# Optimization experiments

Measured on AMD Instinct MI355X. Metric: run time of the kernel, lower is better.

The kernel has to match this reference:

```python
import math
import jax, jax.numpy as jnp
import numpy as np

DN = ('NCHW', 'OIHW', 'NCHW')

def _conv2d(x, w, b, stride, padding='VALID'):
    y = jax.lax.conv_general_dilated(x, w, window_strides=stride, padding=padding,
                                     dimension_numbers=DN)
    return y + b[None, :, None, None]

def _same_padding_conv(x, w, b, s):
    # replicate torch same_padding_conv: ceil-mode SAME padding, then VALID conv
    H, W = x.shape[2], x.shape[3]
    kh, kw = w.shape[2], w.shape[3]
    out_h, out_w = math.ceil(H / s[0]), math.ceil(W / s[1])
    pad_h = max((out_h - 1) * s[0] + kh - H, 0)
    pad_w = max((out_w - 1) * s[1] + kw - W, 0)
    pt, pl = pad_h // 2, pad_w // 2
    x = jnp.pad(x, ((0, 0), (0, 0), (pt, pad_h - pt), (pl, pad_w - pl)))
    return _conv2d(x, w, b, s)

def _leaky(x):
    return jax.nn.leaky_relu(x, negative_slope=0.2)

def setup_inputs() -> dict:
    key = jax.random.key(0)
    ks = jax.random.split(key, 8)
    B, cin, cout, H, W = 2, 16, 24, 384, 1280
    fl = jax.random.normal(ks[0], (B, cin, H, W), jnp.float32)
    fr = jax.random.normal(ks[1], (B, cin, H, W), jnp.float32)
    w_em = jax.random.normal(ks[2], (cout, cin, 4, 4), jnp.float32) * 0.05
    b_em = jax.random.normal(ks[3], (cout,), jnp.float32) * 0.05
    w_rc = jax.random.normal(ks[4], (cout, cout, 1, 1), jnp.float32) * 0.1
    b_rc = jax.random.normal(ks[5], (cout,), jnp.float32) * 0.05
    w_tf = jax.random.normal(ks[6], (13, cout + 1, 1, 1), jnp.float32) * 0.1
    b_tf = jax.random.normal(ks[7], (13,), jnp.float32) * 0.05
    return {'feature_left': fl, 'feature_right': fr, 'max_disp': 64,
            'w_em': w_em, 'b_em': b_em, 'w_rc': w_rc, 'b_rc': b_rc,
            'w_tf': w_tf, 'b_tf': b_tf}

def reference(feature_left, feature_right, max_disp, w_em, b_em, w_rc, b_rc, w_tf, b_tf):
    # left branch: 4x4 conv, stride (4,4), VALID (torch default padding=0)
    fl = _leaky(_conv2d(_leaky(_conv2d(feature_left, w_em, b_em, (4, 4))), w_rc, b_rc, (1, 1)))
    # right branch: same-padding conv with stride (4,1) -> full width retained
    fr = _leaky(_conv2d(_leaky(_same_padding_conv(feature_right, w_em, b_em, (4, 1))), w_rc, b_rc, (1, 1)))
    B, C, Hq, Wq = fl.shape
    Wr = fr.shape[3]
    # clipped gather indices: idx[d, x] = clip(4*x - d + 1, 0, Wr-1)
    d = jnp.arange(max_disp)[:, None]          # [D,1]
    x = jnp.arange(Wq)[None, :]                # [1,Wq]
    idx = jnp.clip(4 * x - d + 1, 0, Wr - 1)   # [D,Wq]
    fr_g = jnp.take(fr, idx, axis=3)           # [B,C,H,D,Wq]
    # L1 cost over channels -> [B,D,H,Wq]
    cost_volume = jnp.sum(jnp.abs(fl[:, :, :, None, :] - fr_g), axis=1).transpose(0, 2, 1, 3)
    cost_f = jnp.min(cost_volume, axis=1, keepdims=True)                  # [B,1,H,Wq]
    d_init = jnp.argmin(cost_volume, axis=1, keepdims=True).astype(fl.dtype)
    p_init = jnp.concatenate([cost_f, fl], axis=1)
    p_init = _leaky(_conv2d(p_init, w_tf, b_tf, (1, 1)))                  # [B,13,H,Wq]
    z = jnp.zeros_like(d_init)
    out = jnp.concatenate([d_init, z, z, p_init], axis=1)                 # [B,16,H,Wq]
    return out, cost_volume
```

## Files before the change

kernel.cpp:

```cpp
#include <hip/hip_runtime.h>

#define B_   2
#define CIN  16
#define HIN  384
#define WIN  1280
#define CO   24
#define HQ   96
#define WL   320
#define WR   1280
#define DMAX 64

__device__ __forceinline__ float lk(float v) { return v >= 0.f ? v : 0.2f * v; }

__global__ __launch_bounds__(256) void k_left(
    const float* __restrict__ x, const float* __restrict__ w_em,
    const float* __restrict__ b_em, const float* __restrict__ w_rc,
    const float* __restrict__ b_rc, float* __restrict__ out)
{
    __shared__ float sw[CO * CIN * 16];
    __shared__ float swt[CO * CO];
    __shared__ float sbe[CO], sbr[CO];
    __shared__ float em[CO * 128];

    for (int i = threadIdx.x; i < CO * CIN * 16; i += 256) sw[i] = w_em[i];
    for (int i = threadIdx.x; i < CO * CO; i += 256) swt[i] = w_rc[(i % CO) * CO + (i / CO)];
    if (threadIdx.x < CO) { sbe[threadIdx.x] = b_em[threadIdx.x]; sbr[threadIdx.x] = b_rc[threadIdx.x]; }
    __syncthreads();

    const int t = threadIdx.x;
    const int half = t >> 7, pxl = t & 127;
    const int obase = half * 12;
    const int flat = blockIdx.x * 128 + pxl;
    const int j = flat % WL, h = (flat / WL) % HQ, b = flat / (WL * HQ);

    float acc[12];
#pragma unroll
    for (int oo = 0; oo < 12; ++oo) acc[oo] = sbe[obase + oo];

    for (int c = 0; c < CIN; ++c) {
#pragma unroll
        for (int kh = 0; kh < 4; ++kh) {
            const float4 v = *(const float4*)(x + ((size_t)(b * CIN + c) * HIN + 4 * h + kh) * WIN + 4 * j);
#pragma unroll
            for (int oo = 0; oo < 12; ++oo) {
                const float4 wv = *(const float4*)&sw[(((obase + oo) * CIN + c) * 4 + kh) * 4];
                acc[oo] += v.x * wv.x + v.y * wv.y + v.z * wv.z + v.w * wv.w;
            }
        }
    }
#pragma unroll
    for (int oo = 0; oo < 12; ++oo) em[(obase + oo) * 128 + pxl] = lk(acc[oo]);
    __syncthreads();

    float acc2[12];
#pragma unroll
    for (int oo = 0; oo < 12; ++oo) acc2[oo] = sbr[obase + oo];
    for (int c = 0; c < CO; ++c) {
        const float in_c = em[c * 128 + pxl];
#pragma unroll
        for (int oo = 0; oo < 12; ++oo) acc2[oo] += in_c * swt[c * CO + obase + oo];
    }
#pragma unroll
    for (int oo = 0; oo < 12; ++oo)
        out[((size_t)(b * CO + obase + oo) * HQ + h) * WL + j] = lk(acc2[oo]);
}

__global__ __launch_bounds__(256) void k_right(
    const float* __restrict__ x, const float* __restrict__ w_em,
    const float* __restrict__ b_em, const float* __restrict__ w_rc,
    const float* __restrict__ b_rc, float* __restrict__ out)
{
    __shared__ float sw[CO * CIN * 16];
    __shared__ float swt[CO * CO];
    __shared__ float sbe[CO], sbr[CO];
    __shared__ float em[CO * 256];

    for (int i = threadIdx.x; i < CO * CIN * 16; i += 256) sw[i] = w_em[i];
    for (int i = threadIdx.x; i < CO * CO; i += 256) swt[i] = w_rc[(i % CO) * CO + (i / CO)];
    if (threadIdx.x < CO) { sbe[threadIdx.x] = b_em[threadIdx.x]; sbr[threadIdx.x] = b_rc[threadIdx.x]; }
    __syncthreads();

    const int t = threadIdx.x;
    const int L = t & 63, quarter = t >> 6;
    const int obase = quarter * 6;
    const int row = blockIdx.x / 5, jbase = (blockIdx.x % 5) * 256;
    const int b = row / HQ, h = row % HQ;

    const bool vm1 = (jbase + 4 * L - 1) >= 0;
    const bool vp4 = (jbase + 4 * L + 4) < WIN;
    const bool vp5 = (jbase + 4 * L + 5) < WIN;
    const int  im1 = 4 * L - 1;
    const int  ip4 = 4 * L + 4;
    const int  ip5 = 4 * L + 5;

    float acc[4][6];
#pragma unroll
    for (int k = 0; k < 4; ++k)
#pragma unroll
        for (int oo = 0; oo < 6; ++oo) acc[k][oo] = sbe[obase + oo];

    for (int c = 0; c < CIN; ++c) {
#pragma unroll
        for (int kh = 0; kh < 4; ++kh) {
            const float* xr = x + ((size_t)(b * CIN + c) * HIN + 4 * h + kh) * WIN + jbase;
            const float4 v = *(const float4*)(xr + 4 * L);
            float in[7];
            in[0] = vm1 ? xr[im1] : 0.f;
            in[1] = v.x; in[2] = v.y; in[3] = v.z; in[4] = v.w;
            in[5] = vp4 ? xr[ip4] : 0.f;
            in[6] = vp5 ? xr[ip5] : 0.f;
#pragma unroll
            for (int oo = 0; oo < 6; ++oo) {
                const float4 wv = *(const float4*)&sw[(((obase + oo) * CIN + c) * 4 + kh) * 4];
#pragma unroll
                for (int k = 0; k < 4; ++k)
                    acc[k][oo] += in[k] * wv.x + in[k + 1] * wv.y + in[k + 2] * wv.z + in[k + 3] * wv.w;
            }
        }
    }
#pragma unroll
    for (int oo = 0; oo < 6; ++oo) {
        float4 st = make_float4(lk(acc[0][oo]), lk(acc[1][oo]), lk(acc[2][oo]), lk(acc[3][oo]));
        *(float4*)&em[(obase + oo) * 256 + 4 * L] = st;
    }
    __syncthreads();

    float acc2[CO];
#pragma unroll
    for (int o = 0; o < CO; ++o) acc2[o] = sbr[o];
    for (int c = 0; c < CO; ++c) {
        const float in_c = em[c * 256 + t];
#pragma unroll
        for (int o = 0; o < CO; ++o) acc2[o] += in_c * swt[c * CO + o];
    }
#pragma unroll
    for (int o = 0; o < CO; ++o)
        out[((size_t)(b * CO + o) * HQ + h) * WR + jbase + t] = lk(acc2[o]);
}

__global__ __launch_bounds__(320) void k_cost(
    const float* __restrict__ fl, const float* __restrict__ fr,
    const float* __restrict__ wtf, const float* __restrict__ btf,
    float* __restrict__ out, float* __restrict__ cost)
{
    __shared__ float frs[4 * 12 * 337];

    const int j = threadIdx.x;
    const int b = blockIdx.x / HQ, h = blockIdx.x % HQ;

    float acc[DMAX];
#pragma unroll
    for (int d = 0; d < DMAX; ++d) acc[d] = 0.f;

    for (int ch = 0; ch < 2; ++ch) {
        const int c0 = ch * 12;
        __syncthreads();
        for (int c = 0; c < 12; ++c) {
            const float* frow = fr + ((size_t)(b * CO + c0 + c) * HQ + h) * WR;
            const float4 v = *(const float4*)(frow + 4 * j);
            frs[(0 * 12 + c) * 337 + j + 16] = v.x;
            frs[(1 * 12 + c) * 337 + j + 16] = v.y;
            frs[(2 * 12 + c) * 337 + j + 16] = v.z;
            frs[(3 * 12 + c) * 337 + j + 16] = v.w;
            if (j >= 1 && j < 64)
                frs[((j & 3) * 12 + c) * 337 + (j >> 2)] = frow[0];
        }
        __syncthreads();

        for (int c = 0; c < 12; ++c) {
            const float flc = fl[((size_t)(b * CO + c0 + c) * HQ + h) * WL + j];
#pragma unroll
            for (int p = 0; p < 4; ++p) {
                const int dp0 = (1 - p) & 3;
                const int q0 = j + ((65 - dp0) >> 2);
                const int abase = (p * 12 + c) * 337 + q0;
#pragma unroll
                for (int i = 0; i < 16; ++i) {
                    const float v = frs[abase - i];
                    acc[dp0 + 4 * i] += fabsf(flc - v);
                }
            }
        }
    }

    float best = acc[0]; int bd = 0;
#pragma unroll
    for (int d = 1; d < DMAX; ++d)
        if (acc[d] < best) { best = acc[d]; bd = d; }

    const size_t cbase = ((size_t)b * DMAX * HQ + h) * WL + j;
#pragma unroll
    for (int d = 0; d < DMAX; ++d)
        cost[cbase + (size_t)d * (HQ * WL)] = acc[d];

    float flr[CO];
#pragma unroll
    for (int c = 0; c < CO; ++c) flr[c] = fl[((size_t)(b * CO + c) * HQ + h) * WL + j];

#pragma unroll
    for (int o = 0; o < 13; ++o) {
        float a = btf[o] + wtf[o * 25] * best;
#pragma unroll
        for (int c = 0; c < CO; ++c) a += wtf[o * 25 + 1 + c] * flr[c];
        out[((size_t)(b * 16 + 3 + o) * HQ + h) * WL + j] = lk(a);
    }
    out[((size_t)(b * 16 + 0) * HQ + h) * WL + j] = (float)bd;
    out[((size_t)(b * 16 + 1) * HQ + h) * WL + j] = 0.f;
    out[((size_t)(b * 16 + 2) * HQ + h) * WL + j] = 0.f;
}

extern "C" void kernel_launch(void* const* d_in, const int* in_sizes, int n_in,
                              void* d_out, int out_size, void* d_ws, size_t ws_size,
                              hipStream_t stream) {
    const float* fl_in = (const float*)d_in[0];
    const float* fr_in = (const float*)d_in[1];
    const float* w_em = (const float*)d_in[3];
    const float* b_em = (const float*)d_in[4];
    const float* w_rc = (const float*)d_in[5];
    const float* b_rc = (const float*)d_in[6];
    const float* w_tf = (const float*)d_in[7];
    const float* b_tf = (const float*)d_in[8];

    float* out  = (float*)d_out;
    float* cost = out + (size_t)B_ * 16 * HQ * WL;

    float* fl_ws = (float*)d_ws;
    float* fr_ws = fl_ws + (size_t)B_ * CO * HQ * WL;

    hipLaunchKernelGGL(k_left,  dim3(480), dim3(256), 0, stream,
                       fl_in, w_em, b_em, w_rc, b_rc, fl_ws);
    hipLaunchKernelGGL(k_right, dim3(960), dim3(256), 0, stream,
                       fr_in, w_em, b_em, w_rc, b_rc, fr_ws);
    hipLaunchKernelGGL(k_cost,  dim3(192), dim3(320), 0, stream,
                       fl_ws, fr_ws, w_tf, b_tf, out, cost);
}
```

Before: 278.0 us.

## Split cost kernel over disparity groups and column chunks; alias conv shared memory

The cost kernel now gives each thread 16 disparities instead of 64 and splits each row into 64-column chunks. This raises the grid from 192 to 960 blocks and cuts per-thread register pressure. A shared-memory argmin reduction then merges the four disparity groups before the 1x1 output conv. In exchange, each chunk redundantly loads some overlapping right-feature columns, and the conv kernels now reuse the weight shared buffer for intermediates to lower LDS use and raise occupancy.

```diff
diff --git a/kernel.cpp b/kernel.cpp
--- a/kernel.cpp
+++ b/kernel.cpp
@@ -17,12 +17,11 @@
     const float* __restrict__ b_em, const float* __restrict__ w_rc,
     const float* __restrict__ b_rc, float* __restrict__ out)
 {
-    __shared__ float sw[CO * CIN * 16];
+    __shared__ float smem[CO * CIN * 16];
     __shared__ float swt[CO * CO];
     __shared__ float sbe[CO], sbr[CO];
-    __shared__ float em[CO * 128];
-
-    for (int i = threadIdx.x; i < CO * CIN * 16; i += 256) sw[i] = w_em[i];
+
+    for (int i = threadIdx.x; i < CO * CIN * 16; i += 256) smem[i] = w_em[i];
     for (int i = threadIdx.x; i < CO * CO; i += 256) swt[i] = w_rc[(i % CO) * CO + (i / CO)];
     if (threadIdx.x < CO) { sbe[threadIdx.x] = b_em[threadIdx.x]; sbr[threadIdx.x] = b_rc[threadIdx.x]; }
     __syncthreads();
@@ -43,20 +42,21 @@
             const float4 v = *(const float4*)(x + ((size_t)(b * CIN + c) * HIN + 4 * h + kh) * WIN + 4 * j);
 #pragma unroll
             for (int oo = 0; oo < 12; ++oo) {
-                const float4 wv = *(const float4*)&sw[(((obase + oo) * CIN + c) * 4 + kh) * 4];
+                const float4 wv = *(const float4*)&smem[(((obase + oo) * CIN + c) * 4 + kh) * 4];
                 acc[oo] += v.x * wv.x + v.y * wv.y + v.z * wv.z + v.w * wv.w;
             }
         }
     }
-#pragma unroll
-    for (int oo = 0; oo < 12; ++oo) em[(obase + oo) * 128 + pxl] = lk(acc[oo]);
+    __syncthreads();
+#pragma unroll
+    for (int oo = 0; oo < 12; ++oo) smem[(obase + oo) * 128 + pxl] = lk(acc[oo]);
     __syncthreads();
 
     float acc2[12];
 #pragma unroll
     for (int oo = 0; oo < 12; ++oo) acc2[oo] = sbr[obase + oo];
     for (int c = 0; c < CO; ++c) {
-        const float in_c = em[c * 128 + pxl];
+        const float in_c = smem[c * 128 + pxl];
 #pragma unroll
         for (int oo = 0; oo < 12; ++oo) acc2[oo] += in_c * swt[c * CO + obase + oo];
     }
@@ -70,12 +70,11 @@
     const float* __restrict__ b_em, const float* __restrict__ w_rc,
     const float* __restrict__ b_rc, float* __restrict__ out)
 {
-    __shared__ float sw[CO * CIN * 16];
+    __shared__ float smem[CO * CIN * 16];
     __shared__ float swt[CO * CO];
     __shared__ float sbe[CO], sbr[CO];
-    __shared__ float em[CO * 256];
-
-    for (int i = threadIdx.x; i < CO * CIN * 16; i += 256) sw[i] = w_em[i];
+
+    for (int i = threadIdx.x; i < CO * CIN * 16; i += 256) smem[i] = w_em[i];
     for (int i = threadIdx.x; i < CO * CO; i += 256) swt[i] = w_rc[(i % CO) * CO + (i / CO)];
     if (threadIdx.x < CO) { sbe[threadIdx.x] = b_em[threadIdx.x]; sbr[threadIdx.x] = b_rc[threadIdx.x]; }
     __syncthreads();
@@ -111,17 +110,18 @@
             in[6] = vp5 ? xr[ip5] : 0.f;
 #pragma unroll
             for (int oo = 0; oo < 6; ++oo) {
-                const float4 wv = *(const float4*)&sw[(((obase + oo) * CIN + c) * 4 + kh) * 4];
+                const float4 wv = *(const float4*)&smem[(((obase + oo) * CIN + c) * 4 + kh) * 4];
 #pragma unroll
                 for (int k = 0; k < 4; ++k)
                     acc[k][oo] += in[k] * wv.x + in[k + 1] * wv.y + in[k + 2] * wv.z + in[k + 3] * wv.w;
             }
         }
     }
+    __syncthreads();
 #pragma unroll
     for (int oo = 0; oo < 6; ++oo) {
         float4 st = make_float4(lk(acc[0][oo]), lk(acc[1][oo]), lk(acc[2][oo]), lk(acc[3][oo]));
-        *(float4*)&em[(obase + oo) * 256 + 4 * L] = st;
+        *(float4*)&smem[(obase + oo) * 256 + 4 * L] = st;
     }
     __syncthreads();
 
@@ -129,7 +129,7 @@
 #pragma unroll
     for (int o = 0; o < CO; ++o) acc2[o] = sbr[o];
     for (int c = 0; c < CO; ++c) {
-        const float in_c = em[c * 256 + t];
+        const float in_c = smem[c * 256 + t];
 #pragma unroll
         for (int o = 0; o < CO; ++o) acc2[o] += in_c * swt[c * CO + o];
     }
@@ -138,75 +138,87 @@
         out[((size_t)(b * CO + o) * HQ + h) * WR + jbase + t] = lk(acc2[o]);
 }
 
-__global__ __launch_bounds__(320) void k_cost(
+__global__ __launch_bounds__(256) void k_cost(
     const float* __restrict__ fl, const float* __restrict__ fr,
     const float* __restrict__ wtf, const float* __restrict__ btf,
     float* __restrict__ out, float* __restrict__ cost)
 {
-    __shared__ float frs[4 * 12 * 337];
-
-    const int j = threadIdx.x;
-    const int b = blockIdx.x / HQ, h = blockIdx.x % HQ;
-
-    float acc[DMAX];
-#pragma unroll
-    for (int d = 0; d < DMAX; ++d) acc[d] = 0.f;
+    __shared__ float frs[4 * 12 * 81];
+    __shared__ float sbest[256];
+    __shared__ int   sbd[256];
+
+    const int t  = threadIdx.x;
+    const int j  = t & 63;
+    const int dq = t >> 6;
+    const int jc = blockIdx.x % 5;
+    const int r  = blockIdx.x / 5;
+    const int h  = r % HQ, b = r / HQ;
+    const int j0 = jc * 64;
+    const int jg = j0 + j;
+    const int colbase = 4 * j0 - 64;
+
+    float acc[16];
+#pragma unroll
+    for (int dl = 0; dl < 16; ++dl) acc[dl] = 0.f;
 
     for (int ch = 0; ch < 2; ++ch) {
         const int c0 = ch * 12;
         __syncthreads();
+        for (int idx = t; idx < 12 * 320; idx += 256) {
+            const int c = idx / 320, cp = idx % 320;
+            const int col = colbase + cp;
+            const float v = fr[((size_t)(b * CO + c0 + c) * HQ + h) * WR + (col > 0 ? col : 0)];
+            frs[((cp & 3) * 12 + c) * 81 + (cp >> 2)] = v;
+        }
+        __syncthreads();
+
         for (int c = 0; c < 12; ++c) {
-            const float* frow = fr + ((size_t)(b * CO + c0 + c) * HQ + h) * WR;
-            const float4 v = *(const float4*)(frow + 4 * j);
-            frs[(0 * 12 + c) * 337 + j + 16] = v.x;
-            frs[(1 * 12 + c) * 337 + j + 16] = v.y;
-            frs[(2 * 12 + c) * 337 + j + 16] = v.z;
-            frs[(3 * 12 + c) * 337 + j + 16] = v.w;
-            if (j >= 1 && j < 64)
-                frs[((j & 3) * 12 + c) * 337 + (j >> 2)] = frow[0];
-        }
-        __syncthreads();
-
-        for (int c = 0; c < 12; ++c) {
-            const float flc = fl[((size_t)(b * CO + c0 + c) * HQ + h) * WL + j];
+            const float flc = fl[((size_t)(b * CO + c0 + c) * HQ + h) * WL + jg];
 #pragma unroll
             for (int p = 0; p < 4; ++p) {
                 const int dp0 = (1 - p) & 3;
-                const int q0 = j + ((65 - dp0) >> 2);
-                const int abase = (p * 12 + c) * 337 + q0;
-#pragma unroll
-                for (int i = 0; i < 16; ++i) {
-                    const float v = frs[abase - i];
-                    acc[dp0 + 4 * i] += fabsf(flc - v);
-                }
+                const int q0 = j - 4 * dq + ((65 - dp0) >> 2);
+                const int abase = (p * 12 + c) * 81 + q0;
+#pragma unroll
+                for (int i = 0; i < 4; ++i)
+                    acc[dp0 + 4 * i] += fabsf(flc - frs[abase - i]);
             }
         }
     }
 
-    float best = acc[0]; int bd = 0;
-#pragma unroll
-    for (int d = 1; d < DMAX; ++d)
-        if (acc[d] < best) { best = acc[d]; bd = d; }
-
-    const size_t cbase = ((size_t)b * DMAX * HQ + h) * WL + j;
-#pragma unroll
-    for (int d = 0; d < DMAX; ++d)
-        cost[cbase + (size_t)d * (HQ * WL)] = acc[d];
-
-    float flr[CO];
-#pragma unroll
-    for (int c = 0; c < CO; ++c) flr[c] = fl[((size_t)(b * CO + c) * HQ + h) * WL + j];
-
-#pragma unroll
-    for (int o = 0; o < 13; ++o) {
-        float a = btf[o] + wtf[o * 25] * best;
-#pragma unroll
-        for (int c = 0; c < CO; ++c) a += wtf[o * 25 + 1 + c] * flr[c];
-        out[((size_t)(b * 16 + 3 + o) * HQ + h) * WL + j] = lk(a);
-    }
-    out[((size_t)(b * 16 + 0) * HQ + h) * WL + j] = (float)bd;
-    out[((size_t)(b * 16 + 1) * HQ + h) * WL + j] = 0.f;
-    out[((size_t)(b * 16 + 2) * HQ + h) * WL + j] = 0.f;
+    const size_t cb0 = ((size_t)(b * DMAX + 16 * dq) * HQ + h) * WL + jg;
+#pragma unroll
+    for (int dl = 0; dl < 16; ++dl)
+        cost[cb0 + (size_t)dl * (HQ * WL)] = acc[dl];
+
+    float best = acc[0]; int bdl = 0;
+#pragma unroll
+    for (int dl = 1; dl < 16; ++dl)
+        if (acc[dl] < best) { best = acc[dl]; bdl = dl; }
+    sbest[t] = best; sbd[t] = 16 * dq + bdl;
+    __syncthreads();
+
+    if (t < 64) {
+        float cur = sbest[j]; int curd = sbd[j];
+#pragma unroll
+        for (int g = 1; g < 4; ++g) {
+            const float v = sbest[g * 64 + j];
+            if (v < cur) { cur = v; curd = sbd[g * 64 + j]; }
+        }
+        float flr[CO];
+#pragma unroll
+        for (int c = 0; c < CO; ++c) flr[c] = fl[((size_t)(b * CO + c) * HQ + h) * WL + jg];
+#pragma unroll
+        for (int o = 0; o < 13; ++o) {
+            float a = btf[o] + wtf[o * 25] * cur;
+#pragma unroll
+            for (int c = 0; c < CO; ++c) a += wtf[o * 25 + 1 + c] * flr[c];
+            out[((size_t)(b * 16 + 3 + o) * HQ + h) * WL + jg] = lk(a);
+        }
+        out[((size_t)(b * 16 + 0) * HQ + h) * WL + jg] = (float)curd;
+        out[((size_t)(b * 16 + 1) * HQ + h) * WL + jg] = 0.f;
+        out[((size_t)(b * 16 + 2) * HQ + h) * WL + jg] = 0.f;
+    }
 }
 
 extern "C" void kernel_launch(void* const* d_in, const int* in_sizes, int n_in,
@@ -231,6 +243,6 @@
                        fl_in, w_em, b_em, w_rc, b_rc, fl_ws);
     hipLaunchKernelGGL(k_right, dim3(960), dim3(256), 0, stream,
                        fr_in, w_em, b_em, w_rc, b_rc, fr_ws);
-    hipLaunchKernelGGL(k_cost,  dim3(192), dim3(320), 0, stream,
+    hipLaunchKernelGGL(k_cost,  dim3(960), dim3(256), 0, stream,
                        fl_ws, fr_ws, w_tf, b_tf, out, cost);
 }
```

Result: faster. 269.3 us (-3.1%).
